# Kernel tuning notes

Measured on AMD Instinct MI355X. Metric: run time of the kernel, lower is better.

## Reference

```python
import jax, jax.numpy as jnp
import numpy as np

FREQ_RES = 100.0 / 256.0
NUM_FILTERS = 6
_CFG = [(0.5, 4.0), (4.0, 8.0), (8.0, 12.0), (12.0, 16.0), (16.0, 24.0), (24.0, 30.0)]
BANDS = [(int(a / FREQ_RES), int(b / FREQ_RES)) for a, b in _CFG]  # (start_bin, end_bin)


def _interp_idx(n_src, n_dst):
    # torch F.interpolate bilinear, align_corners=False, along last dim (T dim is identity since same size)
    j = np.arange(n_dst)
    src = np.maximum((j + 0.5) * n_src / n_dst - 0.5, 0.0)
    x0 = np.floor(src).astype(np.int32)
    x1 = np.minimum(x0 + 1, n_src - 1)
    w = (src - x0).astype(np.float32)
    return x0, x1, w


def _gelu(x):
    return jax.nn.gelu(x, approximate=False)


def _forward(spec, centers, widths, gains, align_w, align_b, fc1_w, fc1_b, fc2_w, fc2_b,
             band_gain, gate_w, gate_b, proj_w, proj_b, bn_gamma, bn_beta, bn_mean, bn_var):
    B, C, T, F = spec.shape
    N = NUM_FILTERS
    band_feats = []
    for i, (s, e) in enumerate(BANDS):
        nb = e - s + 1
        sl = spec[:, :, :, s:e + 1]                       # [B,C,T,nb]
        mu = jax.nn.softplus(centers[i]) + s              # [C,N]
        mu = jnp.clip(mu, s, s + nb - 1)
        std = jnp.clip(jax.nn.softplus(widths[i]) + 1e-3, 0.5, 2.0 * nb / N)
        freqs = jnp.arange(nb, dtype=spec.dtype)          # relative bins [nb]
        g = jnp.exp(-0.5 * ((freqs[None, None, :] - mu[:, :, None]) / std[:, :, None]) ** 2)  # [C,N,nb]
        w = gains[i][:, :, None] * g / (g.sum(-1, keepdims=True) + 1e-6)
        filt = jnp.einsum('bctf,cnf->bctn', sl, w)        # [B,C,T,N]
        aligned = jnp.einsum('bctn,dc->bdtn', filt, align_w[i]) + align_b[i][None, :, None, None]
        band_feats.append(aligned)
    band_stack = jnp.stack(band_feats, axis=1)            # [B,6,C,T,N]
    nb_bands = band_stack.shape[1]
    x = band_stack.reshape(B, nb_bands * C, T, N)
    h = _gelu(jnp.einsum('bktn,ok->botn', x, fc1_w) + fc1_b[None, :, None, None])
    attn = jnp.einsum('botn,ko->bktn', h, fc2_w) + fc2_b[None, :, None, None]
    attn = jax.nn.softmax(attn.reshape(B, nb_bands, C, T, N), axis=1)  # softmax over bands
    band_stack = band_stack * attn * band_gain[None, :, None, None, None]
    enhanced = jnp.zeros_like(spec)
    for i, (s, e) in enumerate(BANDS):
        nb = e - s + 1
        narrow = band_stack[:, i]                         # [B,C,T,N]
        x0, x1, wl = _interp_idx(NUM_FILTERS, nb)
        wl = jnp.asarray(wl, dtype=spec.dtype)
        bf = narrow[..., x0] * (1.0 - wl) + narrow[..., x1] * wl   # [B,C,T,nb]
        enhanced = enhanced.at[:, :, :, s:e + 1].add(bf)
    residual = enhanced - spec
    gate = jax.nn.sigmoid(jnp.einsum('bctf,dc->bdtf', residual, gate_w) + gate_b[None, :, None, None])
    enhanced2 = spec + gate * residual
    y = jnp.einsum('bctf,dc->bdtf', enhanced2, proj_w) + proj_b[None, :, None, None]
    y = (y - bn_mean[None, :, None, None]) / jnp.sqrt(bn_var[None, :, None, None] + 1e-5)
    y = y * bn_gamma[None, :, None, None] + bn_beta[None, :, None, None]
    return _gelu(y)


def setup_inputs() -> dict:
    key = jax.random.key(0)
    ks = jax.random.split(key, 8)
    B, C, T, F, N = 64, 3, 3000, 103, NUM_FILTERS
    spec = jax.random.normal(ks[0], (B, C, T, F), dtype=jnp.float32)
    centers = jnp.stack([jnp.broadcast_to(jnp.linspace(a, b, N, dtype=jnp.float32) / FREQ_RES, (C, N)) for a, b in _CFG])
    widths = jnp.stack([jnp.full((C, N), (b - a) / N / FREQ_RES, dtype=jnp.float32) for a, b in _CFG])
    gains = jnp.ones((6, C, N), jnp.float32)
    align_w = jax.random.normal(ks[1], (6, C, C), dtype=jnp.float32) / np.sqrt(C)
    align_b = jax.random.normal(ks[2], (6, C), dtype=jnp.float32) * 0.02
    inter = 2 * C
    fc1_w = jax.random.normal(ks[3], (inter, 6 * C), dtype=jnp.float32) / np.sqrt(6 * C)
    fc1_b = jnp.zeros((inter,), jnp.float32)
    fc2_w = jax.random.normal(ks[4], (6 * C, inter), dtype=jnp.float32) / np.sqrt(inter)
    fc2_b = jnp.zeros((6 * C,), jnp.float32)
    band_gain = jnp.ones((6,), jnp.float32)
    gate_w = jax.random.normal(ks[5], (C, C), dtype=jnp.float32) / np.sqrt(C)
    gate_b = jnp.zeros((C,), jnp.float32)
    proj_w = jax.random.normal(ks[6], (C, C), dtype=jnp.float32) / np.sqrt(C)
    proj_b = jnp.zeros((C,), jnp.float32)
    bn_gamma = jnp.ones((C,), jnp.float32)
    bn_beta = jnp.zeros((C,), jnp.float32)
    bn_mean = jnp.zeros((C,), jnp.float32)
    bn_var = jnp.ones((C,), jnp.float32)
    return {"spec": spec, "centers": centers, "widths": widths, "gains": gains,
            "align_w": align_w, "align_b": align_b, "fc1_w": fc1_w, "fc1_b": fc1_b,
            "fc2_w": fc2_w, "fc2_b": fc2_b, "band_gain": band_gain,
            "gate_w": gate_w, "gate_b": gate_b, "proj_w": proj_w, "proj_b": proj_b,
            "bn_gamma": bn_gamma, "bn_beta": bn_beta, "bn_mean": bn_mean, "bn_var": bn_var}


def reference(spec, centers, widths, gains, align_w, align_b, fc1_w, fc1_b, fc2_w, fc2_b,
              band_gain, gate_w, gate_b, proj_w, proj_b, bn_gamma, bn_beta, bn_mean, bn_var):
    return _forward(spec, centers, widths, gains, align_w, align_b, fc1_w, fc1_b, fc2_w, fc2_b,
                    band_gain, gate_w, gate_b, proj_w, proj_b, bn_gamma, bn_beta, bn_mean, bn_var)
```

## Files before the change

kernel.cpp:

```cpp
#include <hip/hip_runtime.h>
#include <math.h>

namespace {

constexpr int C_ = 3, T_ = 3000, F_ = 103, NB_ = 6;
constexpr int TT = 20;
constexpr int BS[NB_]  = {1, 10, 20, 30, 40, 61};
constexpr int BNB[NB_] = {10, 11, 11, 11, 22, 16};
constexpr int BOF[NB_] = {0, 10, 21, 32, 43, 65};
constexpr int SPF = 81;
constexpr int WTOT = 81 * 18;

__device__ __forceinline__ float softplus_(float x) {
  return fmaxf(x, 0.0f) + log1pf(expf(-fabsf(x)));
}
__device__ __forceinline__ float sigmoid_(float z) {
  return 1.0f / (1.0f + __expf(-z));
}
__device__ __forceinline__ float gelu_(float x) {
  return x * sigmoid_(1.595769122f * x * (1.0f + 0.044715f * x * x));
}

__global__ __launch_bounds__(256)
void sleepband_kernel(const float* __restrict__ spec,
                      const float* __restrict__ centers,
                      const float* __restrict__ widths,
                      const float* __restrict__ gains,
                      const float* __restrict__ align_w,
                      const float* __restrict__ align_b,
                      const float* __restrict__ fc1_w,
                      const float* __restrict__ fc1_b,
                      const float* __restrict__ fc2_w,
                      const float* __restrict__ fc2_b,
                      const float* __restrict__ band_gain,
                      const float* __restrict__ gate_w,
                      const float* __restrict__ gate_b,
                      const float* __restrict__ proj_w,
                      const float* __restrict__ proj_b,
                      const float* __restrict__ bn_gamma,
                      const float* __restrict__ bn_beta,
                      const float* __restrict__ bn_mean,
                      const float* __restrict__ bn_var,
                      float* __restrict__ out)
{
  __shared__ float sSpec[C_][TT][SPF];
  __shared__ float sBand[TT][109];
  __shared__ float sW[WTOT];
  __shared__ int   sTc[F_ * 5];
  __shared__ float sTw[F_ * 5];
  __shared__ float sAw[54], sAb[18], sF1[108], sF1b[6], sF2[108], sF2b[18],
                   sBg[6], sGw[9], sGb[3], sPw[9], sPb[3], sBnS[3], sBnO[3];

  const int tid = threadIdx.x;
  const int t0  = blockIdx.x * TT;
  const int b   = blockIdx.y;

  const float* specB = spec + (size_t)b * C_ * T_ * F_;
  for (int li = tid; li < C_ * TT * SPF; li += 256) {
    int c   = li / (TT * SPF);
    int rem = li - c * (TT * SPF);
    int tt  = rem / SPF;
    int f   = rem - tt * SPF;
    sSpec[c][tt][f] = specB[(size_t)c * T_ * F_ + (size_t)(t0 + tt) * F_ + f];
  }

  if (tid < 54)  sAw[tid]  = align_w[tid];
  if (tid < 18)  sAb[tid]  = align_b[tid];
  if (tid < 108) sF1[tid]  = fc1_w[tid];
  if (tid < 6)   sF1b[tid] = fc1_b[tid];
  if (tid < 108) sF2[tid]  = fc2_w[tid];
  if (tid < 18)  sF2b[tid] = fc2_b[tid];
  if (tid < 6)   sBg[tid]  = band_gain[tid];
  if (tid < 9)   sGw[tid]  = gate_w[tid];
  if (tid < 3)   sGb[tid]  = gate_b[tid];
  if (tid < 9)   sPw[tid]  = proj_w[tid];
  if (tid < 3)   sPb[tid]  = proj_b[tid];
  if (tid < 3) {
    float sc = bn_gamma[tid] / sqrtf(bn_var[tid] + 1e-5f);
    sBnS[tid] = sc;
    sBnO[tid] = bn_beta[tid] - bn_mean[tid] * sc;
  }

  if (tid < 108) {
    int i = tid / 18;
    int p = tid - i * 18;
    int s = BS[i], nb = BNB[i];
    float mu = softplus_(centers[tid]) + (float)s;
    mu = fminf(fmaxf(mu, (float)s), (float)(s + nb - 1));
    float sd = softplus_(widths[tid]) + 0.001f;
    sd = fminf(fmaxf(sd, 0.5f), 2.0f * (float)nb / 6.0f);
    float sum = 0.0f;
    for (int f = 0; f < nb; ++f) {
      float d = ((float)f - mu) / sd;
      sum += __expf(-0.5f * d * d);
    }
    float sc = gains[tid] / (sum + 1e-6f);
    float* wrow = &sW[BOF[i] * 18 + p * nb];
    for (int f = 0; f < nb; ++f) {
      float d = ((float)f - mu) / sd;
      wrow[f] = sc * __expf(-0.5f * d * d);
    }
  }

  if (tid >= 128 && tid < 128 + F_) {
    int f = tid - 128;
    int col[4] = {0, 0, 0, 0};
    float w[4] = {0.f, 0.f, 0.f, 0.f};
    int k = 0;
    #pragma unroll
    for (int i = 0; i < NB_; ++i) {
      if (f >= BS[i] && f < BS[i] + BNB[i]) {
        int j = f - BS[i];
        float src = fmaxf(((float)j + 0.5f) * 6.0f / (float)BNB[i] - 0.5f, 0.0f);
        float x0f = floorf(src);
        int   x0  = (int)x0f;
        int   x1  = (x0 + 1 > 5) ? 5 : x0 + 1;
        float wl  = src - x0f;
        col[k] = i * 18 + x0; w[k] = 1.0f - wl;
        col[k + 1] = i * 18 + x1; w[k + 1] = wl;
        k += 2;
      }
    }
    #pragma unroll
    for (int k2 = 0; k2 < 4; ++k2) { sTc[f * 5 + k2] = col[k2]; sTw[f * 5 + k2] = w[k2]; }
  }
  __syncthreads();

  for (int task = tid; task < 18 * TT; task += 256) {
    int p  = task / TT;
    int tt = task - p * TT;
    int c  = p / 6;
    int n  = p - c * 6;
    #pragma unroll
    for (int i = 0; i < NB_; ++i) {
      const float* wrow = &sW[BOF[i] * 18 + p * BNB[i]];
      const float* srow = &sSpec[c][tt][BS[i]];
      float acc = 0.0f;
      #pragma unroll
      for (int f = 0; f < BNB[i]; ++f) acc += srow[f] * wrow[f];
      sBand[tt][(i * 3 + c) * 6 + n] = acc;
    }
  }
  __syncthreads();

  if (tid < 6 * TT) {
    int n  = tid / TT;
    int tt = tid - n * TT;
    float al[18];
    #pragma unroll
    for (int i = 0; i < 6; ++i) {
      float f0 = sBand[tt][(i * 3 + 0) * 6 + n];
      float f1 = sBand[tt][(i * 3 + 1) * 6 + n];
      float f2 = sBand[tt][(i * 3 + 2) * 6 + n];
      #pragma unroll
      for (int d = 0; d < 3; ++d)
        al[i * 3 + d] = sAw[i * 9 + d * 3 + 0] * f0 + sAw[i * 9 + d * 3 + 1] * f1 +
                        sAw[i * 9 + d * 3 + 2] * f2 + sAb[i * 3 + d];
    }
    float h[6];
    #pragma unroll
    for (int o = 0; o < 6; ++o) {
      float acc = sF1b[o];
      #pragma unroll
      for (int k = 0; k < 18; ++k) acc += sF1[o * 18 + k] * al[k];
      h[o] = gelu_(acc);
    }
    float at[18];
    #pragma unroll
    for (int k = 0; k < 18; ++k) {
      float acc = sF2b[k];
      #pragma unroll
      for (int o = 0; o < 6; ++o) acc += sF2[k * 6 + o] * h[o];
      at[k] = acc;
    }
    #pragma unroll
    for (int c = 0; c < 3; ++c) {
      float m = at[c];
      #pragma unroll
      for (int i = 1; i < 6; ++i) m = fmaxf(m, at[i * 3 + c]);
      float e[6], ssum = 0.0f;
      #pragma unroll
      for (int i = 0; i < 6; ++i) { e[i] = __expf(at[i * 3 + c] - m); ssum += e[i]; }
      float inv = 1.0f / ssum;
      #pragma unroll
      for (int i = 0; i < 6; ++i)
        sBand[tt][(i * 3 + c) * 6 + n] = al[i * 3 + c] * (e[i] * inv) * sBg[i];
    }
  }
  __syncthreads();

  for (int task = tid; task < TT * F_; task += 256) {
    int tt = task / F_;
    int f  = task - tt * F_;
    const float* brow = &sBand[tt][0];
    float enh0 = 0.0f, enh1 = 0.0f, enh2 = 0.0f;
    #pragma unroll
    for (int k = 0; k < 4; ++k) {
      int   cb = sTc[f * 5 + k];
      float w  = sTw[f * 5 + k];
      enh0 += brow[cb]      * w;
      enh1 += brow[cb + 6]  * w;
      enh2 += brow[cb + 12] * w;
    }
    const size_t gi = (size_t)(t0 + tt) * F_ + f;
    float sv[3] = { specB[gi], specB[(size_t)T_ * F_ + gi], specB[(size_t)2 * T_ * F_ + gi] };
    float rr[3] = { enh0 - sv[0], enh1 - sv[1], enh2 - sv[2] };
    float e2[3];
    #pragma unroll
    for (int d = 0; d < 3; ++d) {
      float gz = sGw[d * 3 + 0] * rr[0] + sGw[d * 3 + 1] * rr[1] + sGw[d * 3 + 2] * rr[2] + sGb[d];
      e2[d] = sv[d] + sigmoid_(gz) * rr[d];
    }
    #pragma unroll
    for (int d = 0; d < 3; ++d) {
      float y = sPw[d * 3 + 0] * e2[0] + sPw[d * 3 + 1] * e2[1] + sPw[d * 3 + 2] * e2[2] + sPb[d];
      y = y * sBnS[d] + sBnO[d];
      out[((size_t)(b * C_ + d) * T_) * F_ + gi] = gelu_(y);
    }
  }
}

}

extern "C" void kernel_launch(void* const* d_in, const int* in_sizes, int n_in,
                              void* d_out, int out_size, void* d_ws, size_t ws_size,
                              hipStream_t stream) {
  (void)n_in; (void)out_size; (void)d_ws; (void)ws_size;
  const int B = in_sizes[0] / (C_ * T_ * F_);
  dim3 grid(T_ / TT, B);
  sleepband_kernel<<<grid, 256, 0, stream>>>(
      (const float*)d_in[0],  (const float*)d_in[1],  (const float*)d_in[2],
      (const float*)d_in[3],  (const float*)d_in[4],  (const float*)d_in[5],
      (const float*)d_in[6],  (const float*)d_in[7],  (const float*)d_in[8],
      (const float*)d_in[9],  (const float*)d_in[10], (const float*)d_in[11],
      (const float*)d_in[12], (const float*)d_in[13], (const float*)d_in[14],
      (const float*)d_in[15], (const float*)d_in[16], (const float*)d_in[17],
      (const float*)d_in[18], (float*)d_out);
}
```

Before: 277.2 us.

## Precompute enhanced rows in shared memory and vectorize the final elementwise pass

Interpolation tables are replaced by a per-(channel,time) pass that writes the full enhanced spectrum row into a reused shared-memory pool, summing the overlapping band endpoints through a carry. The final gating/projection/GELU pass then runs on float4 loads and stores over contiguous t*F ranges, with the small weights hoisted into registers. The aim is to cut the gather overhead and the scalar global traffic in the dominant output loop. It adds another __syncthreads, relies on 16-byte alignment of t0*F offsets (TT*F_=2060 is divisible by 4), and overlays the enhanced rows onto the spec staging buffer.

```diff
diff --git a/kernel.cpp b/kernel.cpp
--- a/kernel.cpp
+++ b/kernel.cpp
@@ -9,7 +9,9 @@
 constexpr int BNB[NB_] = {10, 11, 11, 11, 22, 16};
 constexpr int BOF[NB_] = {0, 10, 21, 32, 43, 65};
 constexpr int SPF = 81;
-constexpr int WTOT = 81 * 18;
+constexpr int PLANE = T_ * F_;
+constexpr int SEC = 2064;
+constexpr int POOLN = 6320;
 
 __device__ __forceinline__ float softplus_(float x) {
   return fmaxf(x, 0.0f) + log1pf(expf(-fabsf(x)));
@@ -43,11 +45,8 @@
                       const float* __restrict__ bn_var,
                       float* __restrict__ out)
 {
-  __shared__ float sSpec[C_][TT][SPF];
+  __shared__ __align__(16) float sPool[POOLN];
   __shared__ float sBand[TT][109];
-  __shared__ float sW[WTOT];
-  __shared__ int   sTc[F_ * 5];
-  __shared__ float sTw[F_ * 5];
   __shared__ float sAw[54], sAb[18], sF1[108], sF1b[6], sF2[108], sF2b[18],
                    sBg[6], sGw[9], sGb[3], sPw[9], sPb[3], sBnS[3], sBnO[3];
 
@@ -55,13 +54,15 @@
   const int t0  = blockIdx.x * TT;
   const int b   = blockIdx.y;
 
-  const float* specB = spec + (size_t)b * C_ * T_ * F_;
+  float* sW = sPool + C_ * TT * SPF;
+
+  const float* specB = spec + (size_t)b * C_ * PLANE;
   for (int li = tid; li < C_ * TT * SPF; li += 256) {
     int c   = li / (TT * SPF);
     int rem = li - c * (TT * SPF);
     int tt  = rem / SPF;
     int f   = rem - tt * SPF;
-    sSpec[c][tt][f] = specB[(size_t)c * T_ * F_ + (size_t)(t0 + tt) * F_ + f];
+    sPool[li] = specB[(size_t)c * PLANE + (size_t)(t0 + tt) * F_ + f];
   }
 
   if (tid < 54)  sAw[tid]  = align_w[tid];
@@ -81,48 +82,26 @@
     sBnO[tid] = bn_beta[tid] - bn_mean[tid] * sc;
   }
 
-  if (tid < 108) {
-    int i = tid / 18;
-    int p = tid - i * 18;
+  if (tid >= 128 && tid < 128 + 108) {
+    int q = tid - 128;
+    int i = q / 18;
+    int p = q - i * 18;
     int s = BS[i], nb = BNB[i];
-    float mu = softplus_(centers[tid]) + (float)s;
+    float mu = softplus_(centers[q]) + (float)s;
     mu = fminf(fmaxf(mu, (float)s), (float)(s + nb - 1));
-    float sd = softplus_(widths[tid]) + 0.001f;
+    float sd = softplus_(widths[q]) + 0.001f;
     sd = fminf(fmaxf(sd, 0.5f), 2.0f * (float)nb / 6.0f);
     float sum = 0.0f;
     for (int f = 0; f < nb; ++f) {
       float d = ((float)f - mu) / sd;
       sum += __expf(-0.5f * d * d);
     }
-    float sc = gains[tid] / (sum + 1e-6f);
+    float sc = gains[q] / (sum + 1e-6f);
     float* wrow = &sW[BOF[i] * 18 + p * nb];
     for (int f = 0; f < nb; ++f) {
       float d = ((float)f - mu) / sd;
       wrow[f] = sc * __expf(-0.5f * d * d);
     }
-  }
-
-  if (tid >= 128 && tid < 128 + F_) {
-    int f = tid - 128;
-    int col[4] = {0, 0, 0, 0};
-    float w[4] = {0.f, 0.f, 0.f, 0.f};
-    int k = 0;
-    #pragma unroll
-    for (int i = 0; i < NB_; ++i) {
-      if (f >= BS[i] && f < BS[i] + BNB[i]) {
-        int j = f - BS[i];
-        float src = fmaxf(((float)j + 0.5f) * 6.0f / (float)BNB[i] - 0.5f, 0.0f);
-        float x0f = floorf(src);
-        int   x0  = (int)x0f;
-        int   x1  = (x0 + 1 > 5) ? 5 : x0 + 1;
-        float wl  = src - x0f;
-        col[k] = i * 18 + x0; w[k] = 1.0f - wl;
-        col[k + 1] = i * 18 + x1; w[k + 1] = wl;
-        k += 2;
-      }
-    }
-    #pragma unroll
-    for (int k2 = 0; k2 < 4; ++k2) { sTc[f * 5 + k2] = col[k2]; sTw[f * 5 + k2] = w[k2]; }
   }
   __syncthreads();
 
@@ -131,10 +110,11 @@
     int tt = task - p * TT;
     int c  = p / 6;
     int n  = p - c * 6;
+    const float* srowb = &sPool[(c * TT + tt) * SPF];
     #pragma unroll
     for (int i = 0; i < NB_; ++i) {
       const float* wrow = &sW[BOF[i] * 18 + p * BNB[i]];
-      const float* srow = &sSpec[c][tt][BS[i]];
+      const float* srow = srowb + BS[i];
       float acc = 0.0f;
       #pragma unroll
       for (int f = 0; f < BNB[i]; ++f) acc += srow[f] * wrow[f];
@@ -189,34 +169,75 @@
   }
   __syncthreads();
 
-  for (int task = tid; task < TT * F_; task += 256) {
-    int tt = task / F_;
-    int f  = task - tt * F_;
-    const float* brow = &sBand[tt][0];
-    float enh0 = 0.0f, enh1 = 0.0f, enh2 = 0.0f;
-    #pragma unroll
-    for (int k = 0; k < 4; ++k) {
-      int   cb = sTc[f * 5 + k];
-      float w  = sTw[f * 5 + k];
-      enh0 += brow[cb]      * w;
-      enh1 += brow[cb + 6]  * w;
-      enh2 += brow[cb + 12] * w;
-    }
-    const size_t gi = (size_t)(t0 + tt) * F_ + f;
-    float sv[3] = { specB[gi], specB[(size_t)T_ * F_ + gi], specB[(size_t)2 * T_ * F_ + gi] };
-    float rr[3] = { enh0 - sv[0], enh1 - sv[1], enh2 - sv[2] };
-    float e2[3];
-    #pragma unroll
-    for (int d = 0; d < 3; ++d) {
-      float gz = sGw[d * 3 + 0] * rr[0] + sGw[d * 3 + 1] * rr[1] + sGw[d * 3 + 2] * rr[2] + sGb[d];
-      e2[d] = sv[d] + sigmoid_(gz) * rr[d];
-    }
-    #pragma unroll
-    for (int d = 0; d < 3; ++d) {
-      float y = sPw[d * 3 + 0] * e2[0] + sPw[d * 3 + 1] * e2[1] + sPw[d * 3 + 2] * e2[2] + sPb[d];
-      y = y * sBnS[d] + sBnO[d];
-      out[((size_t)(b * C_ + d) * T_) * F_ + gi] = gelu_(y);
-    }
+  if (tid < C_ * TT) {
+    const int c  = tid / TT;
+    const int tt = tid - c * TT;
+    float bnd[36];
+    #pragma unroll
+    for (int i = 0; i < 6; ++i)
+      #pragma unroll
+      for (int n = 0; n < 6; ++n)
+        bnd[i * 6 + n] = sBand[tt][(i * 3 + c) * 6 + n];
+    float* row = &sPool[c * SEC + tt * F_];
+    row[0] = 0.0f;
+    float carry = 0.0f;
+    #pragma unroll
+    for (int i = 0; i < NB_; ++i) {
+      #pragma unroll
+      for (int j = 0; j < BNB[i]; ++j) {
+        float src = ((float)j + 0.5f) * 6.0f / (float)BNB[i] - 0.5f;
+        src = src > 0.0f ? src : 0.0f;
+        int   x0 = (int)src;
+        int   x1 = (x0 < 5) ? x0 + 1 : 5;
+        float wl = src - (float)x0;
+        float v  = bnd[i * 6 + x0] * (1.0f - wl) + bnd[i * 6 + x1] * wl;
+        if (j == 0) v += carry;
+        if (i < NB_ - 1 && j == BNB[i] - 1) carry = v;
+        else row[BS[i] + j] = v;
+      }
+    }
+    #pragma unroll
+    for (int f = 77; f < F_; ++f) row[f] = 0.0f;
+  }
+  __syncthreads();
+
+  float gw[9], pw[9], gb3[3], pb3[3], bs3[3], bo3[3];
+  #pragma unroll
+  for (int k = 0; k < 9; ++k) { gw[k] = sGw[k]; pw[k] = sPw[k]; }
+  #pragma unroll
+  for (int k = 0; k < 3; ++k) { gb3[k] = sGb[k]; pb3[k] = sPb[k]; bs3[k] = sBnS[k]; bo3[k] = sBnO[k]; }
+
+  const float* sp0 = specB + (size_t)t0 * F_;
+  float* outB = out + (size_t)b * C_ * PLANE + (size_t)t0 * F_;
+  for (int e4 = tid; e4 < (TT * F_) / 4; e4 += 256) {
+    const int e = e4 * 4;
+    const float4 sA = *(const float4*)(sp0 + e);
+    const float4 sB = *(const float4*)(sp0 + PLANE + e);
+    const float4 sC = *(const float4*)(sp0 + 2 * PLANE + e);
+    const float4 eA = *(const float4*)&sPool[0 * SEC + e];
+    const float4 eB = *(const float4*)&sPool[1 * SEC + e];
+    const float4 eC = *(const float4*)&sPool[2 * SEC + e];
+    float4 oA, oB, oC;
+    const float* sAp = (const float*)&sA; const float* sBp = (const float*)&sB;
+    const float* sCp = (const float*)&sC;
+    const float* eAp = (const float*)&eA; const float* eBp = (const float*)&eB;
+    const float* eCp = (const float*)&eC;
+    float* oAp = (float*)&oA; float* oBp = (float*)&oB; float* oCp = (float*)&oC;
+    #pragma unroll
+    for (int j = 0; j < 4; ++j) {
+      float sv0 = sAp[j], sv1 = sBp[j], sv2 = sCp[j];
+      float r0 = eAp[j] - sv0, r1 = eBp[j] - sv1, r2 = eCp[j] - sv2;
+      float e20 = sv0 + sigmoid_(gw[0] * r0 + gw[1] * r1 + gw[2] * r2 + gb3[0]) * r0;
+      float e21 = sv1 + sigmoid_(gw[3] * r0 + gw[4] * r1 + gw[5] * r2 + gb3[1]) * r1;
+      float e22 = sv2 + sigmoid_(gw[6] * r0 + gw[7] * r1 + gw[8] * r2 + gb3[2]) * r2;
+      float y0 = (pw[0] * e20 + pw[1] * e21 + pw[2] * e22 + pb3[0]) * bs3[0] + bo3[0];
+      float y1 = (pw[3] * e20 + pw[4] * e21 + pw[5] * e22 + pb3[1]) * bs3[1] + bo3[1];
+      float y2 = (pw[6] * e20 + pw[7] * e21 + pw[8] * e22 + pb3[2]) * bs3[2] + bo3[2];
+      oAp[j] = gelu_(y0); oBp[j] = gelu_(y1); oCp[j] = gelu_(y2);
+    }
+    *(float4*)(outB + e) = oA;
+    *(float4*)(outB + PLANE + e) = oB;
+    *(float4*)(outB + 2 * PLANE + e) = oC;
   }
 }
 
```

After: 246.9 us. 1.12x faster.
